# Kernel tuning notes

Hardware: AMD Instinct MI355X
Metric: run time of the kernel (lower is better)

The kernel has to match this reference:

```python
import jax, jax.numpy as jnp
import numpy as np

HEADS = 16
DIM_HEAD = 64


def setup_inputs() -> dict:
    key = jax.random.key(0)
    k1, k2, k3 = jax.random.split(key, 3)
    b, n, dim = 2, 2048, 1024
    x = jax.random.normal(k1, (b, n, dim), dtype=jnp.float32)
    W_qkv = jax.random.normal(k2, (dim, 6 * HEADS * DIM_HEAD), dtype=jnp.float32) * 0.02
    W_out = jax.random.normal(k3, (HEADS * DIM_HEAD, dim), dtype=jnp.float32) * 0.02
    return {"x": x, "W_qkv": W_qkv, "W_out": W_out}


def reference(x, W_qkv, W_out):
    b, n, _ = x.shape
    h, d = HEADS, DIM_HEAD
    scale = d ** -0.5

    # project and split into 6 head-wise tensors: (qkv h d) grouping order
    qkv = (x @ W_qkv).reshape(b, n, 6, h, d).transpose(2, 0, 3, 1, 4)  # [6,b,h,n,d]
    qu, ku, vu, qc, kc, vc = qkv
    qu_s = qu * scale
    qc_s = qc * scale

    idx = jnp.arange(n)
    future = idx[None, :] > idx[:, None]  # torch triu(1): True strictly above diag

    # term1: qc . vu, zeroed on future positions
    term1 = jnp.einsum('bhid,bhjd->bhij', qc_s, vu)
    term1 = jnp.where(future, 0.0, term1)

    # sigmoid lookahead attention, kept ONLY on strictly-future positions
    lookahead = jax.nn.sigmoid(jnp.einsum('bhid,bhjd->bhij', qu_s, ku))
    lookahead = jnp.where(future, lookahead, 0.0)

    # Su[i,k] = sum_j term1[i,j] * lookahead[k,j]
    Su = jnp.einsum('bhij,bhkj->bhik', term1, lookahead)
    Sc = jnp.einsum('bhid,bhjd->bhij', qc_s, kc)

    scores = Sc - jax.nn.silu(Su)
    neg = -jnp.finfo(scores.dtype).max
    scores = jnp.where(future, neg, scores)

    attn = jax.nn.softmax(scores, axis=-1)
    out = jnp.einsum('bhij,bhjd->bhid', attn, vc)  # [b,h,n,d]

    out = out.transpose(0, 2, 1, 3).reshape(b, n, h * d)
    return out @ W_out
```

## Files before the change

kernel.cpp:

```cpp
#include <hip/hip_runtime.h>
#include <hip/hip_bf16.h>
#include <stdint.h>


typedef unsigned short u16;
typedef __attribute__((ext_vector_type(8))) short s8v;
typedef __attribute__((ext_vector_type(4))) float f4v;

__device__ __forceinline__ u16 f2bf(float f) {
  union { float f; unsigned u; } v; v.f = f;
  unsigned r = v.u + 0x7FFFu + ((v.u >> 16) & 1u);
  return (u16)(r >> 16);
}
__device__ __forceinline__ float bf2f(u16 u) {
  union { unsigned u; float f; } v; v.u = ((unsigned)u) << 16; return v.f;
}

typedef __attribute__((address_space(1))) const void* gas_t;
typedef __attribute__((address_space(3))) void* las_t;
__device__ __forceinline__ void gld16(const void* g, void* l) {
  __builtin_amdgcn_global_load_lds((gas_t)g, (las_t)l, 16, 0, 0);
}

__device__ __forceinline__ void zero_acc(f4v acc[4][4]) {
  f4v z = {0.f, 0.f, 0.f, 0.f};
#pragma unroll
  for (int m = 0; m < 4; ++m)
#pragma unroll
    for (int n = 0; n < 4; ++n) acc[m][n] = z;
}


__global__ void convert_x_kernel(const float* __restrict__ in, u16* __restrict__ out) {
  int i = (blockIdx.x * 256 + threadIdx.x) * 4;
  float4 v = *(const float4*)(&in[i]);
  out[i + 0] = f2bf(v.x);
  out[i + 1] = f2bf(v.y);
  out[i + 2] = f2bf(v.z);
  out[i + 3] = f2bf(v.w);
}

__global__ void transpose_convert_kernel(const float* __restrict__ in, u16* __restrict__ out,
                                         int R, int C) {
  __shared__ float tile[32][33];
  int c0 = blockIdx.x * 32, r0 = blockIdx.y * 32;
  for (int rr = threadIdx.y; rr < 32; rr += 8)
    tile[rr][threadIdx.x] = in[(size_t)(r0 + rr) * C + (c0 + threadIdx.x)];
  __syncthreads();
  for (int cc = threadIdx.y; cc < 32; cc += 8)
    out[(size_t)(c0 + cc) * R + (r0 + threadIdx.x)] = f2bf(tile[threadIdx.x][cc]);
}


__global__ __launch_bounds__(256, 2) void gemm_qkv_kernel(
    const u16* __restrict__ xb, const u16* __restrict__ wqkvT,
    u16* __restrict__ quS, u16* __restrict__ ku, u16* __restrict__ vu,
    u16* __restrict__ qcS, u16* __restrict__ kc, u16* __restrict__ vcT) {
  __shared__ u16 sA[2][8192];
  __shared__ u16 sB[2][8192];
  int bm = blockIdx.x, bn = blockIdx.y;
  int tid = threadIdx.x, lane = tid & 63, w = tid >> 6, wm = w >> 1, wn = w & 1;
  int g = lane >> 4, l15 = lane & 15;
  const int sz = (l15 & 7) << 3;
  const int bo = tid * 16;

  const u16* Ab = xb + (size_t)(bm * 128) * 1024;
  const u16* Bb = wqkvT + (size_t)(bn * 128) * 1024;

  auto stg = [&](const u16* base, int ks, u16* dst) {
#pragma unroll
    for (int it = 0; it < 4; ++it) {
      int o = bo + it * 4096;
      int row = o >> 7, lo = o & 127;
      gld16(base + (size_t)row * 1024 + ks * 64 + ((lo ^ ((row & 7) << 4)) >> 1),
            (char*)dst + o);
    }
  };

  f4v acc[4][4];
  zero_acc(acc);
  stg(Ab, 0, sA[0]);
  stg(Bb, 0, sB[0]);
  stg(Ab, 1, sA[1]);
  stg(Bb, 1, sB[1]);

  for (int ks = 0; ks < 16; ++ks) {
    int buf = ks & 1;
    if (ks < 15)
      asm volatile("s_waitcnt vmcnt(8)" ::: "memory");
    else
      asm volatile("s_waitcnt vmcnt(0)" ::: "memory");
    __builtin_amdgcn_sched_barrier(0);
    __builtin_amdgcn_s_barrier();
    __builtin_amdgcn_sched_barrier(0);
#pragma unroll
    for (int kk = 0; kk < 2; ++kk) {
      int c2 = kk * 32 + g * 8;
      s8v a[4], b[4];
#pragma unroll
      for (int m = 0; m < 4; ++m)
        a[m] = *(const s8v*)(&sA[buf][(wm * 64 + m * 16 + l15) * 64 + (c2 ^ sz)]);
#pragma unroll
      for (int n = 0; n < 4; ++n)
        b[n] = *(const s8v*)(&sB[buf][(wn * 64 + n * 16 + l15) * 64 + (c2 ^ sz)]);
#pragma unroll
      for (int m = 0; m < 4; ++m)
#pragma unroll
        for (int n = 0; n < 4; ++n)
          acc[m][n] = __builtin_amdgcn_mfma_f32_16x16x32_bf16(a[m], b[n], acc[m][n], 0, 0, 0);
    }
    __builtin_amdgcn_s_barrier();
    if (ks + 2 < 16) {
      stg(Ab, ks + 2, sA[buf]);
      stg(Bb, ks + 2, sB[buf]);
    }
  }

  int s = bn >> 3;
  int b = bm >> 4;
  int nn0 = (bm & 15) * 128;
  int hh0 = (bn & 7) * 2;
  float scale = (s == 0 || s == 3) ? 0.125f : 1.f;
  u16* sE = (u16*)sA;
  if (s == 5) {
#pragma unroll
    for (int pass = 0; pass < 2; ++pass) {
      __syncthreads();
      if (wn == pass) {
#pragma unroll
        for (int m = 0; m < 4; ++m)
#pragma unroll
          for (int n = 0; n < 4; ++n)
#pragma unroll
            for (int j = 0; j < 4; ++j) {
              int lrow = wm * 64 + m * 16 + g * 4 + j;
              int d = n * 16 + l15;
              sE[lrow * 72 + d] = f2bf(acc[m][n][j]);
            }
      }
      __syncthreads();
      int bh = (b << 4) + hh0 + pass;
      u16* dst = vcT + (size_t)bh * 64 * 2048 + nn0;
      for (int it = 0; it < 4; ++it) {
        int c2 = tid + it * 256;
        int dd2 = c2 >> 4, nseg = c2 & 15;
        u16 tmp[8];
#pragma unroll
        for (int e = 0; e < 8; ++e) tmp[e] = sE[(nseg * 8 + e) * 72 + dd2];
        *(uint4*)(dst + (size_t)dd2 * 2048 + nseg * 8) = *(uint4*)tmp;
      }
    }
  } else {
    u16* obase;
    switch (s) {
      case 0: obase = quS; break;
      case 1: obase = ku; break;
      case 2: obase = vu; break;
      case 3: obase = qcS; break;
      default: obase = kc; break;
    }
#pragma unroll
    for (int pass = 0; pass < 2; ++pass) {
      __syncthreads();
      if (wn == pass) {
#pragma unroll
        for (int m = 0; m < 4; ++m)
#pragma unroll
          for (int n = 0; n < 4; ++n)
#pragma unroll
            for (int j = 0; j < 4; ++j) {
              int lrow = wm * 64 + m * 16 + g * 4 + j;
              int d = n * 16 + l15;
              sE[lrow * 64 + d] = f2bf(acc[m][n][j] * scale);
            }
      }
      __syncthreads();
      int bh = (b << 4) + hh0 + pass;
      u16* dst = obase + ((size_t)bh * 2048 + nn0) * 64;
      for (int it = 0; it < 4; ++it) {
        int e = (tid + it * 256) * 8;
        *(uint4*)(dst + e) = *(const uint4*)(&sE[e]);
      }
    }
  }
}


__global__ __launch_bounds__(256, 2) void tl_kernel(
    const u16* __restrict__ qcS, const u16* __restrict__ vu,
    const u16* __restrict__ quS, const u16* __restrict__ ku,
    u16* __restrict__ term1p, u16* __restrict__ lookp, int c0) {
  __shared__ u16 S[32768];
  int t = blockIdx.x, lb = blockIdx.y, bh = c0 + lb;
  int I = 0;
  while ((I + 1) * (I + 2) / 2 <= t) ++I;
  int K = t - I * (I + 1) / 2;
  int tid = threadIdx.x, lane = tid & 63, w = tid >> 6, wm = w >> 1, wn = w & 1;
  int g = lane >> 4, l15 = lane & 15;
  const int sz = (l15 & 7) << 3;
  const int bo = tid * 16;

  auto stg = [&](const u16* base, int rt, u16* dst) {
#pragma unroll
    for (int it = 0; it < 4; ++it) {
      int o = bo + it * 4096;
      int row = o >> 7, lo = o & 127;
      gld16(base + ((size_t)bh * 2048 + rt * 128 + row) * 64 + ((lo ^ ((row & 7) << 4)) >> 1),
            (char*)dst + o);
    }
  };
  stg(qcS, I, S);
  stg(vu, K, S + 8192);
  stg(quS, K, S + 16384);
  stg(ku, I, S + 24576);

  asm volatile("s_waitcnt vmcnt(0)" ::: "memory");
  __builtin_amdgcn_sched_barrier(0);
  __syncthreads();

  f4v acc1[4][4], acc2[4][4];
  zero_acc(acc1);
  zero_acc(acc2);
#pragma unroll
  for (int kk = 0; kk < 2; ++kk) {
    int c2 = kk * 32 + g * 8;
    s8v a1[4], b1[4], a2[4], b2[4];
#pragma unroll
    for (int m = 0; m < 4; ++m) {
      a1[m] = *(const s8v*)(&S[(wm * 64 + m * 16 + l15) * 64 + (c2 ^ sz)]);
      a2[m] = *(const s8v*)(&S[16384 + (wm * 64 + m * 16 + l15) * 64 + (c2 ^ sz)]);
    }
#pragma unroll
    for (int n = 0; n < 4; ++n) {
      b1[n] = *(const s8v*)(&S[8192 + (wn * 64 + n * 16 + l15) * 64 + (c2 ^ sz)]);
      b2[n] = *(const s8v*)(&S[24576 + (wn * 64 + n * 16 + l15) * 64 + (c2 ^ sz)]);
    }
#pragma unroll
    for (int m = 0; m < 4; ++m)
#pragma unroll
      for (int n = 0; n < 4; ++n) {
        acc1[m][n] = __builtin_amdgcn_mfma_f32_16x16x32_bf16(a1[m], b1[n], acc1[m][n], 0, 0, 0);
        acc2[m][n] = __builtin_amdgcn_mfma_f32_16x16x32_bf16(a2[m], b2[n], acc2[m][n], 0, 0, 0);
      }
  }
  __syncthreads();

#pragma unroll
  for (int m = 0; m < 4; ++m)
#pragma unroll
    for (int n = 0; n < 4; ++n)
#pragma unroll
      for (int j4 = 0; j4 < 4; ++j4) {
        int lr = wm * 64 + m * 16 + g * 4 + j4;
        int lc = wn * 64 + n * 16 + l15;
        int idx = wn * 8192 + lr * 64 + ((lc & 63) ^ ((lr & 7) << 3));
        float v1 = acc1[m][n][j4];
        v1 = ((K * 128 + lc) > (I * 128 + lr)) ? 0.f : v1;
        S[idx] = f2bf(v1);
        float v2 = acc2[m][n][j4];
        v2 = ((I * 128 + lc) > (K * 128 + lr)) ? (1.f / (1.f + __expf(-v2))) : 0.f;
        S[16384 + idx] = f2bf(v2);
      }
  __syncthreads();

  u16* o1 = term1p + ((size_t)lb * 136 + t) * 16384;
  u16* o2 = lookp + ((size_t)lb * 136 + t) * 16384;
#pragma unroll
  for (int it = 0; it < 8; ++it) {
    int e = (tid + it * 256) * 8;
    *(uint4*)(o1 + e) = *(const uint4*)(&S[e]);
    *(uint4*)(o2 + e) = *(const uint4*)(&S[16384 + e]);
  }
}


__global__ __launch_bounds__(256, 2) void castle_kernel(
    const u16* __restrict__ term1p, const u16* __restrict__ lookp,
    const u16* __restrict__ qcS, const u16* __restrict__ kc,
    const u16* __restrict__ vcT,
    u16* __restrict__ opart, float* __restrict__ ml, int c0) {
  __shared__ u16 sA[16384];
  __shared__ u16 sB[16384];
  int bid = blockIdx.x;
  int lb = bid / 136, sid = bid % 136;
  int bh = c0 + lb;
  int I = 15, rem = sid;
  while (rem > I) { rem -= I + 1; --I; }
  int K = rem;
  int t = I * (I + 1) / 2 + K;

  int tid = threadIdx.x, lane = tid & 63, w = tid >> 6;
  int g = lane >> 4, l15 = lane & 15;
  const int sz = (l15 & 7) << 3;

  const char* t1b = (const char*)(term1p + (size_t)lb * 136 * 16384);
  const char* lkb = (const char*)(lookp + (size_t)lb * 136 * 16384);
  const int IT = I * (I + 1) / 2;
  const int bo = tid * 16;

  s8v qa[2][2];
#pragma unroll
  for (int mg = 0; mg < 2; ++mg)
#pragma unroll
    for (int kk = 0; kk < 2; ++kk)
      qa[mg][kk] = *(const s8v*)(&qcS[((size_t)bh * 2048 + I * 128 + w * 32 + mg * 16 + l15) * 64 +
                                      kk * 32 + g * 8]);

  f4v su[2][8];
  {
    f4v z = {0.f, 0.f, 0.f, 0.f};
#pragma unroll
    for (int mg = 0; mg < 2; ++mg)
#pragma unroll
      for (int n = 0; n < 8; ++n) su[mg][n] = z;
  }

  auto stage = [&](const char* sa, const char* sb, int buf) {
    char* dA = (char*)sA + buf * 16384;
    char* dB = (char*)sB + buf * 16384;
#pragma unroll
    for (int it = 0; it < 4; ++it) {
      gld16(sa + bo + it * 4096, dA + bo + it * 4096);
      gld16(sb + bo + it * 4096, dB + bo + it * 4096);
    }
  };

  const char* srcA = t1b + (size_t)(IT + K) * 32768;
  const char* srcB = lkb + (size_t)(K * (K + 1) / 2 + K) * 32768;

  const int h0 = 2 * K, h1 = 2 * I + 1;
  stage(srcA, srcB, 0);
  for (int h = h0; h <= h1; ++h) {
    int cur = (h - h0) & 1;
    if (h < h1) {
      srcA += 16384;
      srcB += (h & 1) ? (((size_t)((h >> 1) + 1) << 15) - 16384) : 16384;
      stage(srcA, srcB, cur ^ 1);
      asm volatile("s_waitcnt vmcnt(8)" ::: "memory");
    } else {
      asm volatile("s_waitcnt vmcnt(0)" ::: "memory");
    }
    __builtin_amdgcn_sched_barrier(0);
    __builtin_amdgcn_s_barrier();
    __builtin_amdgcn_sched_barrier(0);
    const u16* bA = sA + cur * 8192;
    const u16* bB = sB + cur * 8192;
    __builtin_amdgcn_s_setprio(1);
#pragma unroll
    for (int kk = 0; kk < 2; ++kk) {
      int c2 = kk * 32 + g * 8;
      s8v a[2], b[8];
      a[0] = *(const s8v*)(&bA[(w * 32 + l15) * 64 + (c2 ^ sz)]);
      a[1] = *(const s8v*)(&bA[(w * 32 + 16 + l15) * 64 + (c2 ^ sz)]);
#pragma unroll
      for (int n = 0; n < 8; ++n)
        b[n] = *(const s8v*)(&bB[(n * 16 + l15) * 64 + (c2 ^ sz)]);
#pragma unroll
      for (int mg = 0; mg < 2; ++mg)
#pragma unroll
        for (int n = 0; n < 8; ++n)
          su[mg][n] = __builtin_amdgcn_mfma_f32_16x16x32_bf16(a[mg], b[n], su[mg][n], 0, 0, 0);
    }
    __builtin_amdgcn_s_setprio(0);
    __builtin_amdgcn_s_barrier();
  }

  {
#pragma unroll
    for (int it = 0; it < 4; ++it) {
      int o = bo + it * 4096;
      int kh = o >> 13, oc = o & 8191;
      int dr = oc >> 7, lo = oc & 127;
      const u16* src = vcT + ((size_t)bh * 64 + dr) * 2048 + K * 128 + kh * 64 +
                       ((lo ^ ((dr & 7) << 4)) >> 1);
      gld16(src, (char*)sB + o);
    }
#pragma unroll
    for (int it = 0; it < 4; ++it) {
      int o = bo + it * 4096;
      int row = o >> 7, lo = o & 127;
      const u16* src = kc + ((size_t)bh * 2048 + K * 128 + row) * 64 +
                       ((lo ^ ((row & 7) << 4)) >> 1);
      gld16(src, (char*)sB + 16384 + o);
    }
  }
#pragma unroll
  for (int mg = 0; mg < 2; ++mg)
#pragma unroll
    for (int n = 0; n < 8; ++n)
#pragma unroll
      for (int j4 = 0; j4 < 4; ++j4) {
        float xv = su[mg][n][j4];
        su[mg][n][j4] = -(xv / (1.f + __expf(-xv)));
      }
  __syncthreads();

#pragma unroll
  for (int kk = 0; kk < 2; ++kk) {
    int c = kk * 32 + g * 8;
    s8v b[8];
#pragma unroll
    for (int n = 0; n < 8; ++n)
      b[n] = *(const s8v*)(&sB[8192 + (n * 16 + l15) * 64 + (c ^ sz)]);
#pragma unroll
    for (int mg = 0; mg < 2; ++mg)
#pragma unroll
      for (int n = 0; n < 8; ++n)
        su[mg][n] = __builtin_amdgcn_mfma_f32_16x16x32_bf16(qa[mg][kk], b[n], su[mg][n], 0, 0, 0);
  }

  if (K == I) {
#pragma unroll
    for (int mg = 0; mg < 2; ++mg)
#pragma unroll
      for (int n = 0; n < 8; ++n)
#pragma unroll
        for (int j4 = 0; j4 < 4; ++j4) {
          int lr = w * 32 + mg * 16 + g * 4 + j4;
          int lc = n * 16 + l15;
          if (lc > lr) su[mg][n][j4] = -3.0e38f;
        }
  }

  float mrow[2][4], lrow[2][4];
#pragma unroll
  for (int mg = 0; mg < 2; ++mg)
#pragma unroll
    for (int j4 = 0; j4 < 4; ++j4) {
      float v = -3.0e38f;
#pragma unroll
      for (int n = 0; n < 8; ++n) v = fmaxf(v, su[mg][n][j4]);
      v = fmaxf(v, __shfl_xor(v, 1));
      v = fmaxf(v, __shfl_xor(v, 2));
      v = fmaxf(v, __shfl_xor(v, 4));
      v = fmaxf(v, __shfl_xor(v, 8));
      mrow[mg][j4] = v;
    }
#pragma unroll
  for (int mg = 0; mg < 2; ++mg)
#pragma unroll
    for (int j4 = 0; j4 < 4; ++j4) {
      float sum = 0.f;
      int prow = w * 32 + mg * 16 + g * 4 + j4;
      int psz = ((g * 4 + j4) & 7) << 3;
#pragma unroll
      for (int n = 0; n < 8; ++n) {
        float e = __expf(su[mg][n][j4] - mrow[mg][j4]);
        sum += e;
        int pc = n * 16 + l15;
        sA[(n >> 2) * 8192 + prow * 64 + ((pc & 63) ^ psz)] = f2bf(e);
      }
      sum += __shfl_xor(sum, 1);
      sum += __shfl_xor(sum, 2);
      sum += __shfl_xor(sum, 4);
      sum += __shfl_xor(sum, 8);
      lrow[mg][j4] = sum;
    }
  __syncthreads();

  f4v o[2][4];
  {
    f4v z = {0.f, 0.f, 0.f, 0.f};
#pragma unroll
    for (int mg = 0; mg < 2; ++mg)
#pragma unroll
      for (int nd = 0; nd < 4; ++nd) o[mg][nd] = z;
  }
#pragma unroll
  for (int kk = 0; kk < 4; ++kk) {
    int kh = kk >> 1;
    int cc = (kk & 1) * 32 + g * 8;
    s8v pa[2], vb[4];
#pragma unroll
    for (int mg = 0; mg < 2; ++mg)
      pa[mg] = *(const s8v*)(&sA[kh * 8192 + (w * 32 + mg * 16 + l15) * 64 + (cc ^ sz)]);
#pragma unroll
    for (int nd = 0; nd < 4; ++nd)
      vb[nd] = *(const s8v*)(&sB[kh * 4096 + (nd * 16 + l15) * 64 + (cc ^ sz)]);
#pragma unroll
    for (int mg = 0; mg < 2; ++mg)
#pragma unroll
      for (int nd = 0; nd < 4; ++nd)
        o[mg][nd] = __builtin_amdgcn_mfma_f32_16x16x32_bf16(pa[mg], vb[nd], o[mg][nd], 0, 0, 0);
  }

  size_t tb = (size_t)lb * 136 + t;
#pragma unroll
  for (int mg = 0; mg < 2; ++mg)
#pragma unroll
    for (int nd = 0; nd < 4; ++nd)
#pragma unroll
      for (int j4 = 0; j4 < 4; ++j4) {
        int prow = w * 32 + mg * 16 + g * 4 + j4;
        int dcol = nd * 16 + l15;
        opart[(tb * 128 + prow) * 64 + dcol] = f2bf(o[mg][nd][j4]);
      }
  if (l15 == 0) {
#pragma unroll
    for (int mg = 0; mg < 2; ++mg)
#pragma unroll
      for (int j4 = 0; j4 < 4; ++j4) {
        int prow = w * 32 + mg * 16 + g * 4 + j4;
        ml[tb * 256 + prow] = mrow[mg][j4];
        ml[tb * 256 + 128 + prow] = lrow[mg][j4];
      }
  }
}


__global__ __launch_bounds__(256) void combine_kernel(const u16* __restrict__ opart,
                                                      const float* __restrict__ ml,
                                                      u16* __restrict__ attn, int c0) {
  int lb = blockIdx.x, I = blockIdx.y, bh = c0 + lb;
  int tid = threadIdx.x;
  int row = tid >> 1, dh = (tid & 1) << 5;
  float M = -3.0e38f, L = 0.f;
  float O[32];
#pragma unroll
  for (int i = 0; i < 32; ++i) O[i] = 0.f;
  for (int K = 0; K <= I; ++K) {
    size_t tb = (size_t)lb * 136 + I * (I + 1) / 2 + K;
    float m = ml[tb * 256 + row];
    float l = ml[tb * 256 + 128 + row];
    float newM = fmaxf(M, m);
    float so = __expf(M - newM), sn = __expf(m - newM);
    L = L * so + l * sn;
    const u16* op = opart + (tb * 128 + row) * 64 + dh;
#pragma unroll
    for (int q = 0; q < 4; ++q) {
      s8v ov = *(const s8v*)(op + q * 8);
#pragma unroll
      for (int e = 0; e < 8; ++e)
        O[q * 8 + e] = O[q * 8 + e] * so + bf2f((u16)ov[e]) * sn;
    }
    M = newM;
  }
  float inv = 1.f / L;
  int b = bh >> 4, hh = bh & 15;
  u16* dst = attn + ((size_t)b * 2048 + I * 128 + row) * 1024 + hh * 64 + dh;
#pragma unroll
  for (int i = 0; i < 32; ++i) dst[i] = f2bf(O[i] * inv);
}


__global__ __launch_bounds__(256, 2) void gemm_out_kernel(const u16* __restrict__ attn,
                                                          const u16* __restrict__ woutT,
                                                          float* __restrict__ out) {
  __shared__ u16 sA[2][8192];
  __shared__ u16 sB[2][8192];
  int bm = blockIdx.x, bn = blockIdx.y;
  int tid = threadIdx.x, lane = tid & 63, w = tid >> 6, wm = w >> 1, wn = w & 1;
  int g = lane >> 4, l15 = lane & 15;
  const int sz = (l15 & 7) << 3;
  const int bo = tid * 16;

  const u16* Ab = attn + (size_t)(bm * 128) * 1024;
  const u16* Bb = woutT + (size_t)(bn * 128) * 1024;

  auto stg = [&](const u16* base, int ks, u16* dst) {
#pragma unroll
    for (int it = 0; it < 4; ++it) {
      int o = bo + it * 4096;
      int row = o >> 7, lo = o & 127;
      gld16(base + (size_t)row * 1024 + ks * 64 + ((lo ^ ((row & 7) << 4)) >> 1),
            (char*)dst + o);
    }
  };

  f4v acc[4][4];
  zero_acc(acc);
  stg(Ab, 0, sA[0]);
  stg(Bb, 0, sB[0]);
  stg(Ab, 1, sA[1]);
  stg(Bb, 1, sB[1]);

  for (int ks = 0; ks < 16; ++ks) {
    int buf = ks & 1;
    if (ks < 15)
      asm volatile("s_waitcnt vmcnt(8)" ::: "memory");
    else
      asm volatile("s_waitcnt vmcnt(0)" ::: "memory");
    __builtin_amdgcn_sched_barrier(0);
    __builtin_amdgcn_s_barrier();
    __builtin_amdgcn_sched_barrier(0);
#pragma unroll
    for (int kk = 0; kk < 2; ++kk) {
      int c2 = kk * 32 + g * 8;
      s8v a[4], b[4];
#pragma unroll
      for (int m = 0; m < 4; ++m)
        a[m] = *(const s8v*)(&sA[buf][(wm * 64 + m * 16 + l15) * 64 + (c2 ^ sz)]);
#pragma unroll
      for (int n = 0; n < 4; ++n)
        b[n] = *(const s8v*)(&sB[buf][(wn * 64 + n * 16 + l15) * 64 + (c2 ^ sz)]);
#pragma unroll
      for (int m = 0; m < 4; ++m)
#pragma unroll
        for (int n = 0; n < 4; ++n)
          acc[m][n] = __builtin_amdgcn_mfma_f32_16x16x32_bf16(a[m], b[n], acc[m][n], 0, 0, 0);
    }
    __builtin_amdgcn_s_barrier();
    if (ks + 2 < 16) {
      stg(Ab, ks + 2, sA[buf]);
      stg(Bb, ks + 2, sB[buf]);
    }
  }

#pragma unroll
  for (int m = 0; m < 4; ++m)
#pragma unroll
    for (int n = 0; n < 4; ++n)
#pragma unroll
      for (int j = 0; j < 4; ++j) {
        int row = bm * 128 + wm * 64 + m * 16 + g * 4 + j;
        int col = bn * 128 + wn * 64 + n * 16 + l15;
        out[(size_t)row * 1024 + col] = acc[m][n][j];
      }
}


extern "C" void kernel_launch(void* const* d_in, const int* in_sizes, int n_in,
                              void* d_out, int out_size, void* d_ws, size_t ws_size,
                              hipStream_t stream) {
  const float* x = (const float*)d_in[0];
  const float* Wqkv = (const float*)d_in[1];
  const float* Wout = (const float*)d_in[2];
  float* out = (float*)d_out;

  char* base = (char*)d_ws;
  size_t off = 0;
  auto alloc = [&](size_t bytes) -> void* {
    void* p = base + off;
    off += (bytes + 255) & ~(size_t)255;
    return p;
  };

  u16* woutT = (u16*)alloc(1024ull * 1024 * 2);
  u16* quS = (u16*)alloc(32ull * 2048 * 64 * 2);
  u16* ku = (u16*)alloc(32ull * 2048 * 64 * 2);
  u16* vu = (u16*)alloc(32ull * 2048 * 64 * 2);
  u16* qcS = (u16*)alloc(32ull * 2048 * 64 * 2);
  u16* kc = (u16*)alloc(32ull * 2048 * 64 * 2);
  u16* vcT = (u16*)alloc(32ull * 2048 * 64 * 2);
  u16* attn = (u16*)alloc(4096ull * 1024 * 2);

  size_t perBH = 136ull * 16384 * 2 * 2 + 136ull * 128 * 64 * 2 + 136ull * 256 * 4;
  size_t remain = (ws_size > off) ? (ws_size - off) : 0;
  int chunk = (int)(remain / perBH);
  if (chunk < 1) chunk = 1;
  if (chunk > 32) chunk = 32;
  u16* term1p = (u16*)alloc((size_t)chunk * 136 * 16384 * 2);
  u16* lookp = (u16*)alloc((size_t)chunk * 136 * 16384 * 2);
  u16* opart = (u16*)alloc((size_t)chunk * 136 * 8192 * 2);
  float* mlb = (float*)alloc((size_t)chunk * 136 * 256 * 4);

  u16* xb;
  u16* wqkvT;
  if ((size_t)chunk * 136 * 16384 * 2 >= (4096ull + 6144ull) * 1024 * 2) {
    xb = term1p;
    wqkvT = term1p + 4096ull * 1024;
  } else {
    xb = (u16*)alloc(4096ull * 1024 * 2);
    wqkvT = (u16*)alloc(6144ull * 1024 * 2);
  }

  convert_x_kernel<<<4096, 256, 0, stream>>>(x, xb);
  transpose_convert_kernel<<<dim3(192, 32), dim3(32, 8), 0, stream>>>(Wqkv, wqkvT, 1024, 6144);
  transpose_convert_kernel<<<dim3(32, 32), dim3(32, 8), 0, stream>>>(Wout, woutT, 1024, 1024);
  gemm_qkv_kernel<<<dim3(32, 48), 256, 0, stream>>>(xb, wqkvT, quS, ku, vu, qcS, kc, vcT);

  for (int c0 = 0; c0 < 32; c0 += chunk) {
    int nb = (32 - c0 < chunk) ? (32 - c0) : chunk;
    tl_kernel<<<dim3(136, nb), 256, 0, stream>>>(qcS, vu, quS, ku, term1p, lookp, c0);
    castle_kernel<<<dim3(136 * nb), 256, 0, stream>>>(term1p, lookp, qcS, kc, vcT, opart, mlb, c0);
    combine_kernel<<<dim3(nb, 16), 256, 0, stream>>>(opart, mlb, attn, c0);
  }
  gemm_out_kernel<<<dim3(32, 8), 256, 0, stream>>>(attn, woutT, out);
}
```

Baseline: 498.0 us.

## Halve castle_kernel LDS footprint to raise occupancy, drop double buffering

Cuts the castle kernel's shared memory from 64KB to 32KB and raises launch bounds from 2 to 4 blocks per CU. To fit, the Su accumulation loop loses its double-buffered prefetch and now loads then waits each step. K and V^T are restaged into the two buffers, and the P@V stage writes the probability tile to LDS in two halves so each half is consumed before the next is written. More resident blocks should hide memory latency, at the cost of losing intra-block load/compute overlap and possible register pressure under the tighter launch bound.

```diff
diff --git a/kernel.cpp b/kernel.cpp
--- a/kernel.cpp
+++ b/kernel.cpp
@@ -274,13 +274,13 @@
 }
 
 
-__global__ __launch_bounds__(256, 2) void castle_kernel(
+__global__ __launch_bounds__(256, 4) void castle_kernel(
     const u16* __restrict__ term1p, const u16* __restrict__ lookp,
     const u16* __restrict__ qcS, const u16* __restrict__ kc,
     const u16* __restrict__ vcT,
     u16* __restrict__ opart, float* __restrict__ ml, int c0) {
-  __shared__ u16 sA[16384];
-  __shared__ u16 sB[16384];
+  __shared__ u16 sA[8192];
+  __shared__ u16 sB[8192];
   int bid = blockIdx.x;
   int lb = bid / 136, sid = bid % 136;
   int bh = c0 + lb;
@@ -315,46 +315,30 @@
       for (int n = 0; n < 8; ++n) su[mg][n] = z;
   }
 
-  auto stage = [&](const char* sa, const char* sb, int buf) {
-    char* dA = (char*)sA + buf * 16384;
-    char* dB = (char*)sB + buf * 16384;
-#pragma unroll
-    for (int it = 0; it < 4; ++it) {
-      gld16(sa + bo + it * 4096, dA + bo + it * 4096);
-      gld16(sb + bo + it * 4096, dB + bo + it * 4096);
-    }
-  };
-
   const char* srcA = t1b + (size_t)(IT + K) * 32768;
   const char* srcB = lkb + (size_t)(K * (K + 1) / 2 + K) * 32768;
 
   const int h0 = 2 * K, h1 = 2 * I + 1;
-  stage(srcA, srcB, 0);
   for (int h = h0; h <= h1; ++h) {
-    int cur = (h - h0) & 1;
-    if (h < h1) {
-      srcA += 16384;
-      srcB += (h & 1) ? (((size_t)((h >> 1) + 1) << 15) - 16384) : 16384;
-      stage(srcA, srcB, cur ^ 1);
-      asm volatile("s_waitcnt vmcnt(8)" ::: "memory");
-    } else {
-      asm volatile("s_waitcnt vmcnt(0)" ::: "memory");
-    }
+#pragma unroll
+    for (int it = 0; it < 4; ++it) {
+      gld16(srcA + bo + it * 4096, (char*)sA + bo + it * 4096);
+      gld16(srcB + bo + it * 4096, (char*)sB + bo + it * 4096);
+    }
+    asm volatile("s_waitcnt vmcnt(0)" ::: "memory");
     __builtin_amdgcn_sched_barrier(0);
     __builtin_amdgcn_s_barrier();
     __builtin_amdgcn_sched_barrier(0);
-    const u16* bA = sA + cur * 8192;
-    const u16* bB = sB + cur * 8192;
     __builtin_amdgcn_s_setprio(1);
 #pragma unroll
     for (int kk = 0; kk < 2; ++kk) {
       int c2 = kk * 32 + g * 8;
       s8v a[2], b[8];
-      a[0] = *(const s8v*)(&bA[(w * 32 + l15) * 64 + (c2 ^ sz)]);
-      a[1] = *(const s8v*)(&bA[(w * 32 + 16 + l15) * 64 + (c2 ^ sz)]);
+      a[0] = *(const s8v*)(&sA[(w * 32 + l15) * 64 + (c2 ^ sz)]);
+      a[1] = *(const s8v*)(&sA[(w * 32 + 16 + l15) * 64 + (c2 ^ sz)]);
 #pragma unroll
       for (int n = 0; n < 8; ++n)
-        b[n] = *(const s8v*)(&bB[(n * 16 + l15) * 64 + (c2 ^ sz)]);
+        b[n] = *(const s8v*)(&sB[(n * 16 + l15) * 64 + (c2 ^ sz)]);
 #pragma unroll
       for (int mg = 0; mg < 2; ++mg)
 #pragma unroll
@@ -363,9 +347,19 @@
     }
     __builtin_amdgcn_s_setprio(0);
     __builtin_amdgcn_s_barrier();
+    srcA += 16384;
+    srcB += (h & 1) ? (((size_t)((h >> 1) + 1) << 15) - 16384) : 16384;
   }
 
   {
+#pragma unroll
+    for (int it = 0; it < 4; ++it) {
+      int o = bo + it * 4096;
+      int row = o >> 7, lo = o & 127;
+      const u16* src = kc + ((size_t)bh * 2048 + K * 128 + row) * 64 +
+                       ((lo ^ ((row & 7) << 4)) >> 1);
+      gld16(src, (char*)sA + o);
+    }
 #pragma unroll
     for (int it = 0; it < 4; ++it) {
       int o = bo + it * 4096;
@@ -375,14 +369,6 @@
                        ((lo ^ ((dr & 7) << 4)) >> 1);
       gld16(src, (char*)sB + o);
     }
-#pragma unroll
-    for (int it = 0; it < 4; ++it) {
-      int o = bo + it * 4096;
-      int row = o >> 7, lo = o & 127;
-      const u16* src = kc + ((size_t)bh * 2048 + K * 128 + row) * 64 +
-                       ((lo ^ ((row & 7) << 4)) >> 1);
-      gld16(src, (char*)sB + 16384 + o);
-    }
   }
 #pragma unroll
   for (int mg = 0; mg < 2; ++mg)
@@ -401,7 +387,7 @@
     s8v b[8];
 #pragma unroll
     for (int n = 0; n < 8; ++n)
-      b[n] = *(const s8v*)(&sB[8192 + (n * 16 + l15) * 64 + (c ^ sz)]);
+      b[n] = *(const s8v*)(&sA[(n * 16 + l15) * 64 + (c ^ sz)]);
 #pragma unroll
     for (int mg = 0; mg < 2; ++mg)
 #pragma unroll
@@ -435,20 +421,12 @@
       v = fmaxf(v, __shfl_xor(v, 4));
       v = fmaxf(v, __shfl_xor(v, 8));
       mrow[mg][j4] = v;
-    }
-#pragma unroll
-  for (int mg = 0; mg < 2; ++mg)
-#pragma unroll
-    for (int j4 = 0; j4 < 4; ++j4) {
       float sum = 0.f;
-      int prow = w * 32 + mg * 16 + g * 4 + j4;
-      int psz = ((g * 4 + j4) & 7) << 3;
 #pragma unroll
       for (int n = 0; n < 8; ++n) {
-        float e = __expf(su[mg][n][j4] - mrow[mg][j4]);
+        float e = __expf(su[mg][n][j4] - v);
+        su[mg][n][j4] = e;
         sum += e;
-        int pc = n * 16 + l15;
-        sA[(n >> 2) * 8192 + prow * 64 + ((pc & 63) ^ psz)] = f2bf(e);
       }
       sum += __shfl_xor(sum, 1);
       sum += __shfl_xor(sum, 2);
@@ -459,29 +437,39 @@
   __syncthreads();
 
   f4v o[2][4];
-  {
-    f4v z = {0.f, 0.f, 0.f, 0.f};
+  zero_acc(o);
+#pragma unroll
+  for (int kh = 0; kh < 2; ++kh) {
 #pragma unroll
     for (int mg = 0; mg < 2; ++mg)
 #pragma unroll
-      for (int nd = 0; nd < 4; ++nd) o[mg][nd] = z;
-  }
-#pragma unroll
-  for (int kk = 0; kk < 4; ++kk) {
-    int kh = kk >> 1;
-    int cc = (kk & 1) * 32 + g * 8;
-    s8v pa[2], vb[4];
-#pragma unroll
-    for (int mg = 0; mg < 2; ++mg)
-      pa[mg] = *(const s8v*)(&sA[kh * 8192 + (w * 32 + mg * 16 + l15) * 64 + (cc ^ sz)]);
-#pragma unroll
-    for (int nd = 0; nd < 4; ++nd)
-      vb[nd] = *(const s8v*)(&sB[kh * 4096 + (nd * 16 + l15) * 64 + (cc ^ sz)]);
-#pragma unroll
-    for (int mg = 0; mg < 2; ++mg)
+      for (int j4 = 0; j4 < 4; ++j4) {
+        int rl = w * 32 + mg * 16 + g * 4 + j4;
+        int psz = ((g * 4 + j4) & 7) << 3;
+#pragma unroll
+        for (int nn = 0; nn < 4; ++nn) {
+          int pc = nn * 16 + l15;
+          sA[rl * 64 + (pc ^ psz)] = f2bf(su[mg][kh * 4 + nn][j4]);
+        }
+      }
+    asm volatile("s_waitcnt lgkmcnt(0)" ::: "memory");
+    __builtin_amdgcn_sched_barrier(0);
+#pragma unroll
+    for (int kk2 = 0; kk2 < 2; ++kk2) {
+      int cc = kk2 * 32 + g * 8;
+      s8v pa[2], vb[4];
+      pa[0] = *(const s8v*)(&sA[(w * 32 + l15) * 64 + (cc ^ sz)]);
+      pa[1] = *(const s8v*)(&sA[(w * 32 + 16 + l15) * 64 + (cc ^ sz)]);
 #pragma unroll
       for (int nd = 0; nd < 4; ++nd)
-        o[mg][nd] = __builtin_amdgcn_mfma_f32_16x16x32_bf16(pa[mg], vb[nd], o[mg][nd], 0, 0, 0);
+        vb[nd] = *(const s8v*)(&sB[kh * 4096 + (nd * 16 + l15) * 64 + (cc ^ sz)]);
+#pragma unroll
+      for (int mg = 0; mg < 2; ++mg)
+#pragma unroll
+        for (int nd = 0; nd < 4; ++nd)
+          o[mg][nd] = __builtin_amdgcn_mfma_f32_16x16x32_bf16(pa[mg], vb[nd], o[mg][nd], 0, 0, 0);
+    }
+    __builtin_amdgcn_sched_barrier(0);
   }
 
   size_t tb = (size_t)lb * 136 + t;
```

After: 576.2 us. 1.16x slower.
